# Kernel optimization log

Measured on AMD Instinct MI355X. Metric: run time of the kernel, lower is better.

The kernel has to match this reference:

```python
import jax, jax.numpy as jnp
import numpy as np

T, B, I, H = 512, 256, 128, 256

def setup_inputs() -> dict:
    key = jax.random.key(0)
    ks = jax.random.split(key, 8)
    s_ih = 1.0 / np.sqrt(H)
    return {
        "x": jax.random.normal(ks[0], (T, B, I), dtype=jnp.float32),
        "gt": jax.random.uniform(ks[1], (T, B, 1), dtype=jnp.float32),
        "W_ih": jax.random.uniform(ks[2], (3 * H, I), minval=-s_ih, maxval=s_ih, dtype=jnp.float32),
        "W_hh": jax.random.uniform(ks[3], (3 * H, H), minval=-s_ih, maxval=s_ih, dtype=jnp.float32),
        "b_ih": jax.random.uniform(ks[4], (3 * H,), minval=-s_ih, maxval=s_ih, dtype=jnp.float32),
        "b_hh": jax.random.uniform(ks[5], (3 * H,), minval=-s_ih, maxval=s_ih, dtype=jnp.float32),
        "W_dec": jax.random.uniform(ks[6], (1, H), minval=-s_ih, maxval=s_ih, dtype=jnp.float32),
        "b_dec": jax.random.uniform(ks[7], (1,), minval=-s_ih, maxval=s_ih, dtype=jnp.float32),
    }

def reference(x, gt, W_ih, W_hh, b_ih, b_hh, W_dec, b_dec):
    h_dim = W_hh.shape[1]

    def step(h, inp):
        xt, gtt = inp  # xt: [B, I], gtt: [B, 1]
        gi = xt @ W_ih.T + b_ih          # [B, 3H]
        gh = h @ W_hh.T + b_hh           # [B, 3H]
        i_r, i_z, i_n = jnp.split(gi, 3, axis=-1)
        h_r, h_z, h_n = jnp.split(gh, 3, axis=-1)
        r = jax.nn.sigmoid(i_r + h_r)
        z = jax.nn.sigmoid(i_z + h_z)
        n = jnp.tanh(i_n + r * h_n)
        h_new = (1.0 - z) * n + z * h    # [B, H]
        logit = h_new @ W_dec.T + b_dec  # [B, 1]
        # BCE(sigmoid(logit), gt), reduction='sum': stable log-sigmoid form
        loss = -jnp.sum(gtt * jax.nn.log_sigmoid(logit)
                        + (1.0 - gtt) * jax.nn.log_sigmoid(-logit))
        return h_new, loss

    h0 = jnp.zeros((x.shape[1], h_dim), dtype=x.dtype)
    _, losses = jax.lax.scan(step, h0, (x[:-1], gt[1:]))
    return jnp.sum(losses)
```

## Files before the change

### kernel.cpp

```cpp
#include <hip/hip_runtime.h>
#include <hip/hip_bf16.h>


typedef __bf16 bf16x8_t __attribute__((ext_vector_type(8)));
typedef float floatx4_t __attribute__((ext_vector_type(4)));
typedef int intx4_t __attribute__((ext_vector_type(4)));
typedef unsigned int u32;
typedef u32 u32x4_t __attribute__((ext_vector_type(4)));

#define SW 2032.0f
#define SH 127.0f
#define INV_S (1.0f / (127.0f * 2032.0f))
#define NL2E (-1.44269504088896f)
#define CRZ (NL2E * INV_S)
#define CN (2.0f * NL2E * INV_S)

static __device__ inline u32 pack2bf(float a, float b) {
  __bf16 x = (__bf16)a, y = (__bf16)b;
  unsigned short ux = *(unsigned short*)&x, uy = *(unsigned short*)&y;
  return (u32)ux | ((u32)uy << 16);
}

__global__ void prep_kernel(const float* __restrict__ Whh,
                            const float* __restrict__ Wdec,
                            const float* __restrict__ Wih,
                            char* __restrict__ Wq, char* __restrict__ wdq,
                            __bf16* __restrict__ Wihb,
                            float* __restrict__ h_ws, float* __restrict__ out) {
  int idx = blockIdx.x * 256 + threadIdx.x;
  for (int i = idx; i < 768 * 256; i += 65536) {
    int v = (int)rintf(Whh[i] * SW);
    v = v > 127 ? 127 : (v < -127 ? -127 : v);
    Wq[i] = (char)v;
  }
  for (int i = idx; i < 768 * 128; i += 65536) Wihb[i] = (__bf16)Wih[i];
  if (idx < 256) {
    int v = (int)rintf(Wdec[idx] * SW);
    v = v > 127 ? 127 : (v < -127 ? -127 : v);
    wdq[idx] = (char)v;
  }
  if (idx < 65536) h_ws[idx] = 0.f;
  if (idx == 0) out[0] = 0.f;
}

__global__ __launch_bounds__(256) void xconv_kernel(const float* __restrict__ x,
                                                    __bf16* __restrict__ xb) {
  const size_t i = ((size_t)blockIdx.x * 256 + threadIdx.x) * 8;
  floatx4_t a = *(const floatx4_t*)(x + i);
  floatx4_t b = *(const floatx4_t*)(x + i + 4);
  bf16x8_t t;
#pragma unroll
  for (int j = 0; j < 4; ++j) {
    t[j] = (__bf16)a[j];
    t[4 + j] = (__bf16)b[j];
  }
  *(bf16x8_t*)(xb + i) = t;
}

__global__ __launch_bounds__(256) void gemm1_kernel(
    const __bf16* __restrict__ xb,
    const __bf16* __restrict__ Wihb,
    const float* __restrict__ bih, const float* __restrict__ bhh,
    u32* __restrict__ giw) {
  __shared__ __bf16 As[128][144];
  __shared__ __bf16 Bs[128][144];

  const int tid = threadIdx.x;
  const int w = tid >> 6, lane = tid & 63;
  const int q = lane >> 4, nh = lane & 15;
  const int n0 = blockIdx.x * 128;
  const int b0 = blockIdx.y * 128;
  const int wm = w >> 1, wn = w & 1;

  {
    const bf16x8_t* sa = (const bf16x8_t*)(Wihb + (size_t)n0 * 128);
    const bf16x8_t* sb = (const bf16x8_t*)(xb + (size_t)b0 * 128);
    const int rr = tid >> 4, cc = (tid & 15) * 8;
#pragma unroll
    for (int v = 0; v < 8; ++v) {
      *(bf16x8_t*)&As[v * 16 + rr][cc] = sa[v * 256 + tid];
      *(bf16x8_t*)&Bs[v * 16 + rr][cc] = sb[v * 256 + tid];
    }
  }
  __syncthreads();

  floatx4_t acc[4][4];
#pragma unroll
  for (int a = 0; a < 4; ++a)
#pragma unroll
    for (int b = 0; b < 4; ++b)
#pragma unroll
      for (int j = 0; j < 4; ++j) acc[a][b][j] = 0.f;

#pragma unroll
  for (int kk = 0; kk < 4; ++kk) {
    bf16x8_t af[4], bf[4];
#pragma unroll
    for (int mt = 0; mt < 4; ++mt)
      af[mt] = *(const bf16x8_t*)&As[wm * 64 + mt * 16 + nh][kk * 32 + q * 8];
#pragma unroll
    for (int nt = 0; nt < 4; ++nt)
      bf[nt] = *(const bf16x8_t*)&Bs[wn * 64 + nt * 16 + nh][kk * 32 + q * 8];
#pragma unroll
    for (int mt = 0; mt < 4; ++mt)
#pragma unroll
      for (int nt = 0; nt < 4; ++nt)
        acc[mt][nt] = __builtin_amdgcn_mfma_f32_16x16x32_bf16(
            af[mt], bf[nt], acc[mt][nt], 0, 0, 0);
  }

  const int gate = n0 >> 8;
  const float sc = (gate < 2) ? NL2E : (2.0f * NL2E);
  const int wr_base = ((n0 & 255) >> 5) + wm * 2;
#pragma unroll
  for (int a = 0; a < 2; ++a) {
    const int nnA = n0 + wm * 64 + a * 32 + q * 4;
    floatx4_t biasA = *(const floatx4_t*)(bih + nnA);
    floatx4_t biasB = *(const floatx4_t*)(bih + nnA + 16);
    if (gate < 2) {
      floatx4_t c1 = *(const floatx4_t*)(bhh + nnA);
      floatx4_t c2 = *(const floatx4_t*)(bhh + nnA + 16);
#pragma unroll
      for (int j = 0; j < 4; ++j) {
        biasA[j] += c1[j];
        biasB[j] += c2[j];
      }
    }
    const int wrec = wr_base + a;
#pragma unroll
    for (int nt = 0; nt < 4; ++nt) {
      const int bb = b0 + wn * 64 + nt * 16 + nh;
      const int tl = bb >> 8, gg = (bb >> 2) & 63, jb = bb & 3;
      size_t U =
          (((size_t)tl * 64 + gg) * 3 + gate) * 512 + wrec * 64 + jb * 16 + q * 4;
      u32x4_t pv;
#pragma unroll
      for (int j = 0; j < 4; ++j)
        pv[j] = pack2bf((acc[2 * a][nt][j] + biasA[j]) * sc,
                        (acc[2 * a + 1][nt][j] + biasB[j]) * sc);
      *(u32x4_t*)(giw + U) = pv;
    }
  }
}

__global__ __launch_bounds__(512, 2) void rec_kernel(
    const char* __restrict__ Wq,
    const char* __restrict__ wdq,
    const u32* __restrict__ gi,
    const float* __restrict__ gt, const float* __restrict__ bdec,
    const float* __restrict__ bhh, float* __restrict__ h_ws,
    float* __restrict__ out, int t0, int tc) {
  __shared__ char hb[2][4][288];
  __shared__ float logitbuf[2048];

  const int tid = threadIdx.x;
  const int w = tid >> 6, lane = tid & 63;
  const int q = lane >> 4, nh = lane & 15;
  const int g = blockIdx.x;
  const int col0 = w * 32 + nh;
  const int col1 = col0 + 16;

  intx4_t wf[6][4];
#pragma unroll
  for (int c = 0; c < 3; ++c)
#pragma unroll
    for (int ss = 0; ss < 2; ++ss) {
      const int n = c * 256 + w * 32 + ss * 16 + nh;
#pragma unroll
      for (int kb = 0; kb < 4; ++kb)
        wf[c * 2 + ss][kb] =
            *(const intx4_t*)(Wq + (size_t)n * 256 + kb * 64 + q * 16);
    }
  intx4_t wdf[4];
#pragma unroll
  for (int kb = 0; kb < 4; ++kb) {
    intx4_t z = {0, 0, 0, 0};
    intx4_t v = *(const intx4_t*)(wdq + kb * 64 + q * 16);
    wdf[kb] = (nh == 0) ? v : z;
  }

  const float bn20 = 2.0f * NL2E * bhh[512 + col0];
  const float bn21 = 2.0f * NL2E * bhh[512 + col1];
  const float bdec0 = bdec[0];

  if (tid < 256) {
    const int rr = tid >> 6, c0 = (tid & 63) * 4;
    u32 p = 0;
#pragma unroll
    for (int j = 0; j < 4; ++j) {
      int a = (int)rintf(h_ws[(size_t)(g * 4 + rr) * 256 + c0 + j] * SH);
      a = a > 127 ? 127 : (a < -127 ? -127 : a);
      p |= ((u32)(a & 255)) << (8 * j);
    }
    *(u32*)&hb[0][rr][c0] = p;
  }
  float ho0 = h_ws[(size_t)(g * 4 + q) * 256 + col0];
  float ho1 = h_ws[(size_t)(g * 4 + q) * 256 + col1];
  __syncthreads();

  u32 gcur[3], gnxt[3];
  {
    size_t u = ((size_t)g * 3) * 512 + w * 64 + lane;
#pragma unroll
    for (int c = 0; c < 3; ++c) gcur[c] = gi[u + c * 512];
  }

#pragma unroll 1
  for (int t = 0; t < tc; ++t) {
    const int pb = t & 1;
    {
      const int tp = (t + 1 < tc) ? t + 1 : t;
      size_t u = (((size_t)tp * 64 + g) * 3) * 512 + w * 64 + lane;
#pragma unroll
      for (int c = 0; c < 3; ++c) gnxt[c] = gi[u + c * 512];
    }

    intx4_t hbf[4];
#pragma unroll
    for (int kb = 0; kb < 4; ++kb)
      hbf[kb] = *(const intx4_t*)&hb[pb][nh >> 2][kb * 64 + q * 16];

    intx4_t acc[6], facc;
#pragma unroll
    for (int cs = 0; cs < 6; ++cs)
#pragma unroll
      for (int j = 0; j < 4; ++j) acc[cs][j] = 0;
#pragma unroll
    for (int j = 0; j < 4; ++j) facc[j] = 0;

#pragma unroll
    for (int kb = 0; kb < 4; ++kb) {
#pragma unroll
      for (int cs = 0; cs < 6; ++cs)
        acc[cs] = __builtin_amdgcn_mfma_i32_16x16x64_i8(hbf[kb], wf[cs][kb],
                                                        acc[cs], 0, 0, 0);
      if (w == 0)
        facc = __builtin_amdgcn_mfma_i32_16x16x64_i8(hbf[kb], wdf[kb], facc,
                                                     0, 0, 0);
    }

    const float gr0 = __uint_as_float(gcur[0] << 16);
    const float gr1 = __uint_as_float(gcur[0] & 0xffff0000u);
    const float gz0 = __uint_as_float(gcur[1] << 16);
    const float gz1 = __uint_as_float(gcur[1] & 0xffff0000u);
    const float an0 = __uint_as_float(gcur[2] << 16);
    const float an1 = __uint_as_float(gcur[2] & 0xffff0000u);

    float rr0 = __builtin_amdgcn_rcpf(
        1.f + __builtin_amdgcn_exp2f((float)acc[0][0] * CRZ + gr0));
    float rr1 = __builtin_amdgcn_rcpf(
        1.f + __builtin_amdgcn_exp2f((float)acc[1][0] * CRZ + gr1));
    float zz0 = __builtin_amdgcn_rcpf(
        1.f + __builtin_amdgcn_exp2f((float)acc[2][0] * CRZ + gz0));
    float zz1 = __builtin_amdgcn_rcpf(
        1.f + __builtin_amdgcn_exp2f((float)acc[3][0] * CRZ + gz1));
    float hn20 = (float)acc[4][0] * CN + bn20;
    float hn21 = (float)acc[5][0] * CN + bn21;
    float tv0 = 2.f * __builtin_amdgcn_rcpf(
                          1.f + __builtin_amdgcn_exp2f(rr0 * hn20 + an0)) -
                1.f;
    float tv1 = 2.f * __builtin_amdgcn_rcpf(
                          1.f + __builtin_amdgcn_exp2f(rr1 * hn21 + an1)) -
                1.f;
    float hnew0 = tv0 + zz0 * (ho0 - tv0);
    float hnew1 = tv1 + zz1 * (ho1 - tv1);
    ho0 = hnew0;
    ho1 = hnew1;
    int h0 = (int)rintf(hnew0 * SH);
    int h1 = (int)rintf(hnew1 * SH);
    hb[1 - pb][q][col0] = (char)h0;
    hb[1 - pb][q][col1] = (char)h1;

    if (w == 0 && nh == 0 && t >= 1)
      logitbuf[(t - 1) * 4 + q] = (float)facc[0] * INV_S + bdec0;
    __syncthreads();
#pragma unroll
    for (int c = 0; c < 3; ++c) gcur[c] = gnxt[c];
  }

  if (w == 0) {
    intx4_t fac2 = {0, 0, 0, 0};
#pragma unroll
    for (int kb = 0; kb < 4; ++kb) {
      intx4_t b = *(const intx4_t*)&hb[tc & 1][nh >> 2][kb * 64 + q * 16];
      fac2 = __builtin_amdgcn_mfma_i32_16x16x64_i8(b, wdf[kb], fac2, 0, 0, 0);
    }
    if (nh == 0) logitbuf[(tc - 1) * 4 + q] = (float)fac2[0] * INV_S + bdec0;
  }
  __syncthreads();

  float loss = 0.f;
  for (int i = tid; i < tc * 4; i += 512) {
    float l = logitbuf[i];
    float gtv = gt[(size_t)(t0 + (i >> 2) + 1) * 256 + g * 4 + (i & 3)];
    float t1 = log1pf(__expf(-fabsf(l)));
    loss += gtv * (fmaxf(-l, 0.f) + t1) + (1.f - gtv) * (fmaxf(l, 0.f) + t1);
  }
  loss += __shfl_xor(loss, 1);
  loss += __shfl_xor(loss, 2);
  loss += __shfl_xor(loss, 4);
  loss += __shfl_xor(loss, 8);
  loss += __shfl_xor(loss, 16);
  loss += __shfl_xor(loss, 32);
  if (lane == 0) atomicAdd(out, loss);

  h_ws[(size_t)(g * 4 + q) * 256 + col0] = ho0;
  h_ws[(size_t)(g * 4 + q) * 256 + col1] = ho1;
}

extern "C" void kernel_launch(void* const* d_in, const int* in_sizes, int n_in,
                              void* d_out, int out_size, void* d_ws,
                              size_t ws_size, hipStream_t stream) {
  const float* x = (const float*)d_in[0];
  const float* gt = (const float*)d_in[1];
  const float* Wih = (const float*)d_in[2];
  const float* Whh = (const float*)d_in[3];
  const float* bih = (const float*)d_in[4];
  const float* bhh = (const float*)d_in[5];
  const float* Wdec = (const float*)d_in[6];
  const float* bdec = (const float*)d_in[7];
  float* out = (float*)d_out;

  char* ws = (char*)d_ws;
  char* Wq = ws;
  char* wdq = ws + 196608;
  float* h_ws = (float*)(ws + 197120);
  __bf16* Wihb = (__bf16*)(ws + 459264);
  char* dyn = ws + 655872;
  const size_t per_step = (size_t)393216 + 65536;
  size_t avail = ws_size > 655872 ? ws_size - 655872 : per_step;
  int Tc = (int)(avail / per_step);
  if (Tc < 1) Tc = 1;
  if (Tc > 511) Tc = 511;
  __bf16* xb = (__bf16*)dyn;
  u32* gi = (u32*)(dyn + (size_t)Tc * 65536);

  prep_kernel<<<256, 256, 0, stream>>>(Whh, Wdec, Wih, Wq, wdq, Wihb, h_ws,
                                       out);
  for (int t0 = 0; t0 < 511; t0 += Tc) {
    const int tc = (511 - t0 < Tc) ? (511 - t0) : Tc;
    xconv_kernel<<<tc * 16, 256, 0, stream>>>(x + (size_t)t0 * 256 * 128, xb);
    gemm1_kernel<<<dim3(6, tc * 2), 256, 0, stream>>>(xb, Wihb, bih, bhh, gi);
    rec_kernel<<<64, 512, 0, stream>>>(Wq, wdq, gi, gt, bdec, bhh, h_ws, out,
                                       t0, tc);
  }
}
```

Measured before the change: 533.7 us.

## Fuse input GEMM and recurrence into producer/consumer kernel with chunk counters

Merges the input-projection GEMM and the recurrent loop into one launch. Blocks 0-63 run the GRU recurrence and blocks 64-255 produce gate pre-activations tile by tile, publishing progress through per-chunk atomic counters that consumers poll before entering each 16-step chunk. This lets the input GEMM overlap with the serial recurrence and removes the chunked multi-launch loop and the hidden-state round trip through global memory. It also swaps the per-step __syncthreads for a raw LDS-wait plus barrier. It relies on all 256 blocks being co-resident to avoid deadlock, and it assumes the workspace is large enough for the full gate buffer.

```diff
diff --git a/kernel.cpp b/kernel.cpp
--- a/kernel.cpp
+++ b/kernel.cpp
@@ -15,6 +15,11 @@
 #define CRZ (NL2E * INV_S)
 #define CN (2.0f * NL2E * INV_S)
 
+#define CH_STEPS 16
+#define N_CHUNK 32
+#define N_PROD 192
+#define N_TILE (511 * 12)
+
 static __device__ inline u32 pack2bf(float a, float b) {
   __bf16 x = (__bf16)a, y = (__bf16)b;
   unsigned short ux = *(unsigned short*)&x, uy = *(unsigned short*)&y;
@@ -25,8 +30,8 @@
                             const float* __restrict__ Wdec,
                             const float* __restrict__ Wih,
                             char* __restrict__ Wq, char* __restrict__ wdq,
-                            __bf16* __restrict__ Wihb,
-                            float* __restrict__ h_ws, float* __restrict__ out) {
+                            __bf16* __restrict__ Wihb, u32* __restrict__ cnt,
+                            float* __restrict__ out) {
   int idx = blockIdx.x * 256 + threadIdx.x;
   for (int i = idx; i < 768 * 256; i += 65536) {
     int v = (int)rintf(Whh[i] * SW);
@@ -39,7 +44,7 @@
     v = v > 127 ? 127 : (v < -127 ? -127 : v);
     wdq[idx] = (char)v;
   }
-  if (idx < 65536) h_ws[idx] = 0.f;
+  if (idx < N_CHUNK) cnt[idx] = 0;
   if (idx == 0) out[0] = 0.f;
 }
 
@@ -57,103 +62,111 @@
   *(bf16x8_t*)(xb + i) = t;
 }
 
-__global__ __launch_bounds__(256) void gemm1_kernel(
-    const __bf16* __restrict__ xb,
-    const __bf16* __restrict__ Wihb,
-    const float* __restrict__ bih, const float* __restrict__ bhh,
-    u32* __restrict__ giw) {
-  __shared__ __bf16 As[128][144];
-  __shared__ __bf16 Bs[128][144];
-
-  const int tid = threadIdx.x;
-  const int w = tid >> 6, lane = tid & 63;
-  const int q = lane >> 4, nh = lane & 15;
-  const int n0 = blockIdx.x * 128;
-  const int b0 = blockIdx.y * 128;
-  const int wm = w >> 1, wn = w & 1;
-
-  {
-    const bf16x8_t* sa = (const bf16x8_t*)(Wihb + (size_t)n0 * 128);
-    const bf16x8_t* sb = (const bf16x8_t*)(xb + (size_t)b0 * 128);
-    const int rr = tid >> 4, cc = (tid & 15) * 8;
-#pragma unroll
-    for (int v = 0; v < 8; ++v) {
-      *(bf16x8_t*)&As[v * 16 + rr][cc] = sa[v * 256 + tid];
-      *(bf16x8_t*)&Bs[v * 16 + rr][cc] = sb[v * 256 + tid];
-    }
-  }
-  __syncthreads();
-
-  floatx4_t acc[4][4];
-#pragma unroll
-  for (int a = 0; a < 4; ++a)
-#pragma unroll
-    for (int b = 0; b < 4; ++b)
-#pragma unroll
-      for (int j = 0; j < 4; ++j) acc[a][b][j] = 0.f;
-
-#pragma unroll
-  for (int kk = 0; kk < 4; ++kk) {
-    bf16x8_t af[4], bf[4];
-#pragma unroll
-    for (int mt = 0; mt < 4; ++mt)
-      af[mt] = *(const bf16x8_t*)&As[wm * 64 + mt * 16 + nh][kk * 32 + q * 8];
-#pragma unroll
-    for (int nt = 0; nt < 4; ++nt)
-      bf[nt] = *(const bf16x8_t*)&Bs[wn * 64 + nt * 16 + nh][kk * 32 + q * 8];
-#pragma unroll
-    for (int mt = 0; mt < 4; ++mt)
-#pragma unroll
-      for (int nt = 0; nt < 4; ++nt)
-        acc[mt][nt] = __builtin_amdgcn_mfma_f32_16x16x32_bf16(
-            af[mt], bf[nt], acc[mt][nt], 0, 0, 0);
-  }
-
-  const int gate = n0 >> 8;
-  const float sc = (gate < 2) ? NL2E : (2.0f * NL2E);
-  const int wr_base = ((n0 & 255) >> 5) + wm * 2;
-#pragma unroll
-  for (int a = 0; a < 2; ++a) {
-    const int nnA = n0 + wm * 64 + a * 32 + q * 4;
-    floatx4_t biasA = *(const floatx4_t*)(bih + nnA);
-    floatx4_t biasB = *(const floatx4_t*)(bih + nnA + 16);
-    if (gate < 2) {
-      floatx4_t c1 = *(const floatx4_t*)(bhh + nnA);
-      floatx4_t c2 = *(const floatx4_t*)(bhh + nnA + 16);
-#pragma unroll
-      for (int j = 0; j < 4; ++j) {
-        biasA[j] += c1[j];
-        biasB[j] += c2[j];
-      }
-    }
-    const int wrec = wr_base + a;
-#pragma unroll
-    for (int nt = 0; nt < 4; ++nt) {
-      const int bb = b0 + wn * 64 + nt * 16 + nh;
-      const int tl = bb >> 8, gg = (bb >> 2) & 63, jb = bb & 3;
-      size_t U =
-          (((size_t)tl * 64 + gg) * 3 + gate) * 512 + wrec * 64 + jb * 16 + q * 4;
-      u32x4_t pv;
-#pragma unroll
-      for (int j = 0; j < 4; ++j)
-        pv[j] = pack2bf((acc[2 * a][nt][j] + biasA[j]) * sc,
-                        (acc[2 * a + 1][nt][j] + biasB[j]) * sc);
-      *(u32x4_t*)(giw + U) = pv;
-    }
-  }
-}
-
-__global__ __launch_bounds__(512, 2) void rec_kernel(
+__global__ __launch_bounds__(512, 2) void fused_kernel(
     const char* __restrict__ Wq,
     const char* __restrict__ wdq,
-    const u32* __restrict__ gi,
+    u32* __restrict__ gi,
     const float* __restrict__ gt, const float* __restrict__ bdec,
-    const float* __restrict__ bhh, float* __restrict__ h_ws,
-    float* __restrict__ out, int t0, int tc) {
-  __shared__ char hb[2][4][288];
-  __shared__ float logitbuf[2048];
-
+    const float* __restrict__ bhh, const float* __restrict__ bih,
+    const __bf16* __restrict__ Wihb,
+    const __bf16* __restrict__ xb,
+    u32* __restrict__ cnt, float* __restrict__ out) {
+  __shared__ __align__(16) char smem[90112];
   const int tid = threadIdx.x;
+
+  if (blockIdx.x >= 64) {
+    __bf16(*As)[144] = (__bf16(*)[144])smem;
+    __bf16(*Bs)[144] = (__bf16(*)[144])(smem + 36864);
+    const int j = blockIdx.x - 64;
+    const int w = tid >> 6, lane = tid & 63;
+    const int q = lane >> 4, nh = lane & 15;
+    const int wm = w & 1, wn = w >> 1;
+
+    for (int tile = j; tile < N_TILE; tile += N_PROD) {
+      const int t = tile / 12;
+      const int s = tile - t * 12;
+      const int n0 = (s >> 1) * 128;
+      const int b0 = (s & 1) * 128;
+
+      const bf16x8_t* sa = (const bf16x8_t*)(Wihb + (size_t)n0 * 128);
+      const bf16x8_t* sb = (const bf16x8_t*)(xb + ((size_t)t * 256 + b0) * 128);
+#pragma unroll
+      for (int k = 0; k < 4; ++k) {
+        const int ch = k * 512 + tid;
+        *(bf16x8_t*)&As[ch >> 4][(ch & 15) * 8] = sa[ch];
+        *(bf16x8_t*)&Bs[ch >> 4][(ch & 15) * 8] = sb[ch];
+      }
+      __syncthreads();
+
+      floatx4_t acc[4][2];
+#pragma unroll
+      for (int a = 0; a < 4; ++a)
+#pragma unroll
+        for (int b = 0; b < 2; ++b)
+#pragma unroll
+          for (int jj = 0; jj < 4; ++jj) acc[a][b][jj] = 0.f;
+
+#pragma unroll
+      for (int kk = 0; kk < 4; ++kk) {
+        bf16x8_t af[4], bf[2];
+#pragma unroll
+        for (int mt = 0; mt < 4; ++mt)
+          af[mt] = *(const bf16x8_t*)&As[wm * 64 + mt * 16 + nh][kk * 32 + q * 8];
+#pragma unroll
+        for (int nt = 0; nt < 2; ++nt)
+          bf[nt] = *(const bf16x8_t*)&Bs[wn * 32 + nt * 16 + nh][kk * 32 + q * 8];
+#pragma unroll
+        for (int mt = 0; mt < 4; ++mt)
+#pragma unroll
+          for (int nt = 0; nt < 2; ++nt)
+            acc[mt][nt] = __builtin_amdgcn_mfma_f32_16x16x32_bf16(
+                af[mt], bf[nt], acc[mt][nt], 0, 0, 0);
+      }
+
+      const int gate = n0 >> 8;
+      const float sc = (gate < 2) ? NL2E : (2.0f * NL2E);
+      const int wr_base = ((n0 & 255) >> 5) + wm * 2;
+#pragma unroll
+      for (int a = 0; a < 2; ++a) {
+        const int nnA = n0 + wm * 64 + a * 32 + q * 4;
+        floatx4_t biasA = *(const floatx4_t*)(bih + nnA);
+        floatx4_t biasB = *(const floatx4_t*)(bih + nnA + 16);
+        if (gate < 2) {
+          floatx4_t c1 = *(const floatx4_t*)(bhh + nnA);
+          floatx4_t c2 = *(const floatx4_t*)(bhh + nnA + 16);
+#pragma unroll
+          for (int jj = 0; jj < 4; ++jj) {
+            biasA[jj] += c1[jj];
+            biasB[jj] += c2[jj];
+          }
+        }
+        const int wrec = wr_base + a;
+#pragma unroll
+        for (int nt = 0; nt < 2; ++nt) {
+          const int bb = b0 + wn * 32 + nt * 16 + nh;
+          const int gg = (bb >> 2) & 63, jb = bb & 3;
+          size_t U = (((size_t)t * 64 + gg) * 3 + gate) * 512 + wrec * 64 +
+                     jb * 16 + q * 4;
+          u32x4_t pv;
+#pragma unroll
+          for (int jj = 0; jj < 4; ++jj)
+            pv[jj] = pack2bf((acc[2 * a][nt][jj] + biasA[jj]) * sc,
+                             (acc[2 * a + 1][nt][jj] + biasB[jj]) * sc);
+          *(u32x4_t*)(gi + U) = pv;
+        }
+      }
+      __threadfence();
+      __syncthreads();
+      if (tid == 0)
+        __hip_atomic_fetch_add(&cnt[t >> 4], 1u, __ATOMIC_RELEASE,
+                               __HIP_MEMORY_SCOPE_AGENT);
+    }
+    return;
+  }
+
+  char(*hb)[4][288] = (char(*)[4][288])smem;
+  float* logitbuf = (float*)(smem + 2304);
+
   const int w = tid >> 6, lane = tid & 63;
   const int q = lane >> 4, nh = lane & 15;
   const int g = blockIdx.x;
@@ -183,19 +196,18 @@
   const float bn21 = 2.0f * NL2E * bhh[512 + col1];
   const float bdec0 = bdec[0];
 
-  if (tid < 256) {
-    const int rr = tid >> 6, c0 = (tid & 63) * 4;
-    u32 p = 0;
-#pragma unroll
-    for (int j = 0; j < 4; ++j) {
-      int a = (int)rintf(h_ws[(size_t)(g * 4 + rr) * 256 + c0 + j] * SH);
-      a = a > 127 ? 127 : (a < -127 ? -127 : a);
-      p |= ((u32)(a & 255)) << (8 * j);
-    }
-    *(u32*)&hb[0][rr][c0] = p;
-  }
-  float ho0 = h_ws[(size_t)(g * 4 + q) * 256 + col0];
-  float ho1 = h_ws[(size_t)(g * 4 + q) * 256 + col1];
+  for (int i2 = tid; i2 < 576; i2 += 512) ((u32*)smem)[i2] = 0;
+  float ho0 = 0.f, ho1 = 0.f;
+
+  if (tid == 0) {
+    while (__hip_atomic_load(&cnt[0], __ATOMIC_ACQUIRE,
+                             __HIP_MEMORY_SCOPE_AGENT) < 192u)
+      __builtin_amdgcn_s_sleep(1);
+    while (__hip_atomic_load(&cnt[1], __ATOMIC_ACQUIRE,
+                             __HIP_MEMORY_SCOPE_AGENT) < 192u)
+      __builtin_amdgcn_s_sleep(1);
+    __threadfence();
+  }
   __syncthreads();
 
   u32 gcur[3], gnxt[3];
@@ -205,94 +217,112 @@
     for (int c = 0; c < 3; ++c) gcur[c] = gi[u + c * 512];
   }
 
+  int t = 0;
 #pragma unroll 1
-  for (int t = 0; t < tc; ++t) {
-    const int pb = t & 1;
-    {
-      const int tp = (t + 1 < tc) ? t + 1 : t;
-      size_t u = (((size_t)tp * 64 + g) * 3) * 512 + w * 64 + lane;
-#pragma unroll
-      for (int c = 0; c < 3; ++c) gnxt[c] = gi[u + c * 512];
-    }
-
-    intx4_t hbf[4];
-#pragma unroll
-    for (int kb = 0; kb < 4; ++kb)
-      hbf[kb] = *(const intx4_t*)&hb[pb][nh >> 2][kb * 64 + q * 16];
-
-    intx4_t acc[6], facc;
-#pragma unroll
-    for (int cs = 0; cs < 6; ++cs)
-#pragma unroll
-      for (int j = 0; j < 4; ++j) acc[cs][j] = 0;
-#pragma unroll
-    for (int j = 0; j < 4; ++j) facc[j] = 0;
-
-#pragma unroll
-    for (int kb = 0; kb < 4; ++kb) {
+  for (int c = 0; c < N_CHUNK; ++c) {
+    const int te = (c == N_CHUNK - 1) ? 511 : (c + 1) * CH_STEPS;
+#pragma unroll 1
+    for (; t < te; ++t) {
+      const int pb = t & 1;
+      {
+        const int tp = (t + 1 < 511) ? t + 1 : t;
+        size_t u = (((size_t)tp * 64 + g) * 3) * 512 + w * 64 + lane;
+#pragma unroll
+        for (int cc = 0; cc < 3; ++cc) gnxt[cc] = gi[u + cc * 512];
+      }
+
+      intx4_t hbf[4];
+#pragma unroll
+      for (int kb = 0; kb < 4; ++kb)
+        hbf[kb] = *(const intx4_t*)&hb[pb][nh >> 2][kb * 64 + q * 16];
+
+      intx4_t acc[6], facc;
 #pragma unroll
       for (int cs = 0; cs < 6; ++cs)
-        acc[cs] = __builtin_amdgcn_mfma_i32_16x16x64_i8(hbf[kb], wf[cs][kb],
-                                                        acc[cs], 0, 0, 0);
-      if (w == 0)
-        facc = __builtin_amdgcn_mfma_i32_16x16x64_i8(hbf[kb], wdf[kb], facc,
-                                                     0, 0, 0);
-    }
-
-    const float gr0 = __uint_as_float(gcur[0] << 16);
-    const float gr1 = __uint_as_float(gcur[0] & 0xffff0000u);
-    const float gz0 = __uint_as_float(gcur[1] << 16);
-    const float gz1 = __uint_as_float(gcur[1] & 0xffff0000u);
-    const float an0 = __uint_as_float(gcur[2] << 16);
-    const float an1 = __uint_as_float(gcur[2] & 0xffff0000u);
-
-    float rr0 = __builtin_amdgcn_rcpf(
-        1.f + __builtin_amdgcn_exp2f((float)acc[0][0] * CRZ + gr0));
-    float rr1 = __builtin_amdgcn_rcpf(
-        1.f + __builtin_amdgcn_exp2f((float)acc[1][0] * CRZ + gr1));
-    float zz0 = __builtin_amdgcn_rcpf(
-        1.f + __builtin_amdgcn_exp2f((float)acc[2][0] * CRZ + gz0));
-    float zz1 = __builtin_amdgcn_rcpf(
-        1.f + __builtin_amdgcn_exp2f((float)acc[3][0] * CRZ + gz1));
-    float hn20 = (float)acc[4][0] * CN + bn20;
-    float hn21 = (float)acc[5][0] * CN + bn21;
-    float tv0 = 2.f * __builtin_amdgcn_rcpf(
-                          1.f + __builtin_amdgcn_exp2f(rr0 * hn20 + an0)) -
-                1.f;
-    float tv1 = 2.f * __builtin_amdgcn_rcpf(
-                          1.f + __builtin_amdgcn_exp2f(rr1 * hn21 + an1)) -
-                1.f;
-    float hnew0 = tv0 + zz0 * (ho0 - tv0);
-    float hnew1 = tv1 + zz1 * (ho1 - tv1);
-    ho0 = hnew0;
-    ho1 = hnew1;
-    int h0 = (int)rintf(hnew0 * SH);
-    int h1 = (int)rintf(hnew1 * SH);
-    hb[1 - pb][q][col0] = (char)h0;
-    hb[1 - pb][q][col1] = (char)h1;
-
-    if (w == 0 && nh == 0 && t >= 1)
-      logitbuf[(t - 1) * 4 + q] = (float)facc[0] * INV_S + bdec0;
-    __syncthreads();
-#pragma unroll
-    for (int c = 0; c < 3; ++c) gcur[c] = gnxt[c];
+#pragma unroll
+        for (int jj = 0; jj < 4; ++jj) acc[cs][jj] = 0;
+#pragma unroll
+      for (int jj = 0; jj < 4; ++jj) facc[jj] = 0;
+
+#pragma unroll
+      for (int kb = 0; kb < 4; ++kb) {
+#pragma unroll
+        for (int cs = 0; cs < 6; ++cs)
+          acc[cs] = __builtin_amdgcn_mfma_i32_16x16x64_i8(hbf[kb], wf[cs][kb],
+                                                          acc[cs], 0, 0, 0);
+        if (w == 0)
+          facc = __builtin_amdgcn_mfma_i32_16x16x64_i8(hbf[kb], wdf[kb], facc,
+                                                       0, 0, 0);
+      }
+
+      const float gr0 = __uint_as_float(gcur[0] << 16);
+      const float gr1 = __uint_as_float(gcur[0] & 0xffff0000u);
+      const float gz0 = __uint_as_float(gcur[1] << 16);
+      const float gz1 = __uint_as_float(gcur[1] & 0xffff0000u);
+      const float an0 = __uint_as_float(gcur[2] << 16);
+      const float an1 = __uint_as_float(gcur[2] & 0xffff0000u);
+
+      float rr0 = __builtin_amdgcn_rcpf(
+          1.f + __builtin_amdgcn_exp2f((float)acc[0][0] * CRZ + gr0));
+      float rr1 = __builtin_amdgcn_rcpf(
+          1.f + __builtin_amdgcn_exp2f((float)acc[1][0] * CRZ + gr1));
+      float zz0 = __builtin_amdgcn_rcpf(
+          1.f + __builtin_amdgcn_exp2f((float)acc[2][0] * CRZ + gz0));
+      float zz1 = __builtin_amdgcn_rcpf(
+          1.f + __builtin_amdgcn_exp2f((float)acc[3][0] * CRZ + gz1));
+      float hn20 = (float)acc[4][0] * CN + bn20;
+      float hn21 = (float)acc[5][0] * CN + bn21;
+      float tv0 = 2.f * __builtin_amdgcn_rcpf(
+                            1.f + __builtin_amdgcn_exp2f(rr0 * hn20 + an0)) -
+                  1.f;
+      float tv1 = 2.f * __builtin_amdgcn_rcpf(
+                            1.f + __builtin_amdgcn_exp2f(rr1 * hn21 + an1)) -
+                  1.f;
+      float hnew0 = tv0 + zz0 * (ho0 - tv0);
+      float hnew1 = tv1 + zz1 * (ho1 - tv1);
+      ho0 = hnew0;
+      ho1 = hnew1;
+      int h0 = (int)rintf(hnew0 * SH);
+      int h1 = (int)rintf(hnew1 * SH);
+      hb[1 - pb][q][col0] = (char)h0;
+      hb[1 - pb][q][col1] = (char)h1;
+
+      if (w == 0 && nh == 0 && t >= 1)
+        logitbuf[(t - 1) * 4 + q] = (float)facc[0] * INV_S + bdec0;
+
+      asm volatile("s_waitcnt lgkmcnt(0)" ::: "memory");
+      __builtin_amdgcn_s_barrier();
+      asm volatile("" ::: "memory");
+#pragma unroll
+      for (int cc = 0; cc < 3; ++cc) gcur[cc] = gnxt[cc];
+    }
+    if (c + 2 < N_CHUNK) {
+      const u32 tg = (c + 2 == N_CHUNK - 1) ? 180u : 192u;
+      if (tid == 0) {
+        while (__hip_atomic_load(&cnt[c + 2], __ATOMIC_ACQUIRE,
+                                 __HIP_MEMORY_SCOPE_AGENT) < tg)
+          __builtin_amdgcn_s_sleep(1);
+        __threadfence();
+      }
+      __syncthreads();
+    }
   }
 
   if (w == 0) {
     intx4_t fac2 = {0, 0, 0, 0};
 #pragma unroll
     for (int kb = 0; kb < 4; ++kb) {
-      intx4_t b = *(const intx4_t*)&hb[tc & 1][nh >> 2][kb * 64 + q * 16];
+      intx4_t b = *(const intx4_t*)&hb[1][nh >> 2][kb * 64 + q * 16];
       fac2 = __builtin_amdgcn_mfma_i32_16x16x64_i8(b, wdf[kb], fac2, 0, 0, 0);
     }
-    if (nh == 0) logitbuf[(tc - 1) * 4 + q] = (float)fac2[0] * INV_S + bdec0;
+    if (nh == 0) logitbuf[510 * 4 + q] = (float)fac2[0] * INV_S + bdec0;
   }
   __syncthreads();
 
   float loss = 0.f;
-  for (int i = tid; i < tc * 4; i += 512) {
+  for (int i = tid; i < 511 * 4; i += 512) {
     float l = logitbuf[i];
-    float gtv = gt[(size_t)(t0 + (i >> 2) + 1) * 256 + g * 4 + (i & 3)];
+    float gtv = gt[(size_t)((i >> 2) + 1) * 256 + g * 4 + (i & 3)];
     float t1 = log1pf(__expf(-fabsf(l)));
     loss += gtv * (fmaxf(-l, 0.f) + t1) + (1.f - gtv) * (fmaxf(l, 0.f) + t1);
   }
@@ -303,9 +333,6 @@
   loss += __shfl_xor(loss, 16);
   loss += __shfl_xor(loss, 32);
   if (lane == 0) atomicAdd(out, loss);
-
-  h_ws[(size_t)(g * 4 + q) * 256 + col0] = ho0;
-  h_ws[(size_t)(g * 4 + q) * 256 + col1] = ho1;
 }
 
 extern "C" void kernel_launch(void* const* d_in, const int* in_sizes, int n_in,
@@ -324,24 +351,14 @@
   char* ws = (char*)d_ws;
   char* Wq = ws;
   char* wdq = ws + 196608;
-  float* h_ws = (float*)(ws + 197120);
-  __bf16* Wihb = (__bf16*)(ws + 459264);
-  char* dyn = ws + 655872;
-  const size_t per_step = (size_t)393216 + 65536;
-  size_t avail = ws_size > 655872 ? ws_size - 655872 : per_step;
-  int Tc = (int)(avail / per_step);
-  if (Tc < 1) Tc = 1;
-  if (Tc > 511) Tc = 511;
-  __bf16* xb = (__bf16*)dyn;
-  u32* gi = (u32*)(dyn + (size_t)Tc * 65536);
-
-  prep_kernel<<<256, 256, 0, stream>>>(Whh, Wdec, Wih, Wq, wdq, Wihb, h_ws,
+  u32* cnt = (u32*)(ws + 197120);
+  __bf16* Wihb = (__bf16*)(ws + 197632);
+  __bf16* xb = (__bf16*)(ws + 394240);
+  u32* gi = (u32*)(ws + 33883136);
+
+  prep_kernel<<<256, 256, 0, stream>>>(Whh, Wdec, Wih, Wq, wdq, Wihb, cnt,
                                        out);
-  for (int t0 = 0; t0 < 511; t0 += Tc) {
-    const int tc = (511 - t0 < Tc) ? (511 - t0) : Tc;
-    xconv_kernel<<<tc * 16, 256, 0, stream>>>(x + (size_t)t0 * 256 * 128, xb);
-    gemm1_kernel<<<dim3(6, tc * 2), 256, 0, stream>>>(xb, Wihb, bih, bhh, gi);
-    rec_kernel<<<64, 512, 0, stream>>>(Wq, wdq, gi, gt, bdec, bhh, h_ws, out,
-                                       t0, tc);
-  }
-}
+  xconv_kernel<<<8176, 256, 0, stream>>>(x, xb);
+  fused_kernel<<<256, 512, 0, stream>>>(Wq, wdq, gi, gt, bdec, bhh, bih, Wihb,
+                                        xb, cnt, out);
+}
```

Measured after the change: 1.942 ms. 264% more time.

## Unroll recurrence by two with ping-pong gate prefetch and lighter barrier

Applied to the files above, without the earlier changes.

Unrolls the time loop by two and alternates between two register sets for the precomputed input gates. Each set is refilled two steps ahead, right after it is consumed, which removes the per-step register copy and gives global loads more time to land. Replaces __syncthreads with an explicit LDS-only wait plus s_barrier, so outstanding global prefetches need not drain at every step. The cost is more register pressure and reliance on hand-written waitcnt being correct.

```diff
diff --git a/kernel.cpp b/kernel.cpp
--- a/kernel.cpp
+++ b/kernel.cpp
@@ -198,35 +198,44 @@
   float ho1 = h_ws[(size_t)(g * 4 + q) * 256 + col1];
   __syncthreads();
 
-  u32 gcur[3], gnxt[3];
+  const int tcm1 = tc - 1;
+  u32 GA[3], GB[3];
   {
-    size_t u = ((size_t)g * 3) * 512 + w * 64 + lane;
-#pragma unroll
-    for (int c = 0; c < 3; ++c) gcur[c] = gi[u + c * 512];
-  }
-
-#pragma unroll 1
-  for (int t = 0; t < tc; ++t) {
-    const int pb = t & 1;
-    {
-      const int tp = (t + 1 < tc) ? t + 1 : t;
-      size_t u = (((size_t)tp * 64 + g) * 3) * 512 + w * 64 + lane;
-#pragma unroll
-      for (int c = 0; c < 3; ++c) gnxt[c] = gi[u + c * 512];
-    }
-
+    size_t u0 = ((size_t)g * 3) * 512 + w * 64 + lane;
+#pragma unroll
+    for (int c = 0; c < 3; ++c) GA[c] = gi[u0 + c * 512];
+    const int t1 = tc > 1 ? 1 : 0;
+    size_t u1 = (((size_t)t1 * 64 + g) * 3) * 512 + w * 64 + lane;
+#pragma unroll
+    for (int c = 0; c < 3; ++c) GB[c] = gi[u1 + c * 512];
+  }
+
+  auto STEP = [&](int T, u32* G, int TPRE) {
+    const int pb = T & 1;
     intx4_t hbf[4];
 #pragma unroll
     for (int kb = 0; kb < 4; ++kb)
       hbf[kb] = *(const intx4_t*)&hb[pb][nh >> 2][kb * 64 + q * 16];
 
+    const float gr0 = __uint_as_float(G[0] << 16);
+    const float gr1 = __uint_as_float(G[0] & 0xffff0000u);
+    const float gz0 = __uint_as_float(G[1] << 16);
+    const float gz1 = __uint_as_float(G[1] & 0xffff0000u);
+    const float an0 = __uint_as_float(G[2] << 16);
+    const float an1 = __uint_as_float(G[2] & 0xffff0000u);
+    {
+      size_t up = (((size_t)TPRE * 64 + g) * 3) * 512 + w * 64 + lane;
+#pragma unroll
+      for (int c = 0; c < 3; ++c) G[c] = gi[up + c * 512];
+    }
+
     intx4_t acc[6], facc;
 #pragma unroll
     for (int cs = 0; cs < 6; ++cs)
 #pragma unroll
-      for (int j = 0; j < 4; ++j) acc[cs][j] = 0;
-#pragma unroll
-    for (int j = 0; j < 4; ++j) facc[j] = 0;
+      for (int jj = 0; jj < 4; ++jj) acc[cs][jj] = 0;
+#pragma unroll
+    for (int jj = 0; jj < 4; ++jj) facc[jj] = 0;
 
 #pragma unroll
     for (int kb = 0; kb < 4; ++kb) {
@@ -238,13 +247,6 @@
         facc = __builtin_amdgcn_mfma_i32_16x16x64_i8(hbf[kb], wdf[kb], facc,
                                                      0, 0, 0);
     }
-
-    const float gr0 = __uint_as_float(gcur[0] << 16);
-    const float gr1 = __uint_as_float(gcur[0] & 0xffff0000u);
-    const float gz0 = __uint_as_float(gcur[1] << 16);
-    const float gz1 = __uint_as_float(gcur[1] & 0xffff0000u);
-    const float an0 = __uint_as_float(gcur[2] << 16);
-    const float an1 = __uint_as_float(gcur[2] & 0xffff0000u);
 
     float rr0 = __builtin_amdgcn_rcpf(
         1.f + __builtin_amdgcn_exp2f((float)acc[0][0] * CRZ + gr0));
@@ -271,12 +273,21 @@
     hb[1 - pb][q][col0] = (char)h0;
     hb[1 - pb][q][col1] = (char)h1;
 
-    if (w == 0 && nh == 0 && t >= 1)
-      logitbuf[(t - 1) * 4 + q] = (float)facc[0] * INV_S + bdec0;
-    __syncthreads();
-#pragma unroll
-    for (int c = 0; c < 3; ++c) gcur[c] = gnxt[c];
-  }
+    if (w == 0 && nh == 0 && T >= 1)
+      logitbuf[(T - 1) * 4 + q] = (float)facc[0] * INV_S + bdec0;
+
+    asm volatile("s_waitcnt lgkmcnt(0)" ::: "memory");
+    __builtin_amdgcn_s_barrier();
+    asm volatile("" ::: "memory");
+  };
+
+  int t = 0;
+#pragma unroll 1
+  for (; t + 1 < tc; t += 2) {
+    STEP(t, GA, (t + 2 <= tcm1) ? t + 2 : tcm1);
+    STEP(t + 1, GB, (t + 3 <= tcm1) ? t + 3 : tcm1);
+  }
+  if (t < tc) STEP(t, GA, tcm1);
 
   if (w == 0) {
     intx4_t fac2 = {0, 0, 0, 0};
```

After: 518.6 us. 1.03x faster.
